# Optimization experiments

Hardware: AMD Instinct MI355X
Metric: run time of the kernel (lower is better)

Reference implementation:

```python
import jax, jax.numpy as jnp
import numpy as np

B, N, F_IN, H, F = 2, 2048, 128, 8, 32  # FH = 256, a has 2F = 64


def setup_inputs() -> dict:
    key = jax.random.key(0)
    k_g, k_x, k_w, k_a = jax.random.split(key, 4)
    # sparse-ish adjacency with self loops (float mask, as in the keras code)
    u = jax.random.uniform(k_g, (B, N, N), dtype=jnp.float32)
    g = jnp.maximum((u < 0.05).astype(jnp.float32), jnp.eye(N, dtype=jnp.float32)[None])
    x = jax.random.normal(k_x, (B, N, F_IN), dtype=jnp.float32)
    w = jax.random.normal(k_w, (F_IN, F * H), dtype=jnp.float32) * (1.0 / np.sqrt(F_IN))
    a = jax.random.normal(k_a, (2 * F,), dtype=jnp.float32) * 0.1
    return {"g": g, "x": x, "w": w, "a": a, "n_heads": H}


def reference(g, x, w, a, n_heads):
    # g: [B,N,N] adjacency, x: [B,N,F_in], w: [F_in, F*H], a: [2F]
    Bd, Nd, _ = g.shape
    Fh = w.shape[1] // n_heads
    # linear transform + split heads: xh[b,n,h,f] == (x@w)[b,n, f + Fh*h]
    xh = jnp.dot(x, w).reshape(Bd, Nd, n_heads, Fh)  # [B,N,H,F]
    a1, a2 = a[:Fh], a[Fh:]
    # concat-attention is linear: score[b,i,j,h] = a1.x_j + a2.x_i
    s_j = jnp.einsum('bnhf,f->bnh', xh, a1)  # contribution of the tiled-over-axis1 copy (_x1 -> node j)
    s_i = jnp.einsum('bnhf,f->bnh', xh, a2)  # contribution of _x2 -> node i
    scores = s_i[:, :, None, :] + s_j[:, None, :, :]  # [B,N,N,H]
    e = jnp.exp(jax.nn.leaky_relu(scores, negative_slope=0.2))
    # normalize by sum over neighbors j masked by adjacency (keepdims like K.sum(..., keepdims=True))
    norm = jnp.sum(e * g[..., None], axis=2, keepdims=True)  # [B,N,1,H]
    return e / norm
```

## Files before the change

kernel.cpp:

```cpp
#include <hip/hip_runtime.h>

constexpr int Bv  = 2;
constexpr int Nv  = 2048;
constexpr int FIN = 128;
constexpr int Hn  = 8;
constexpr int Fv  = 32;
constexpr int NROW = Bv * Nv;
constexpr int S    = NROW * Hn;

typedef float v4f __attribute__((ext_vector_type(4)));

__global__ __launch_bounds__(256) void prep_kernel(
    const float* __restrict__ w, const float* __restrict__ a,
    const float* __restrict__ x, float* __restrict__ pq) {
    __shared__ float wa[2 * FIN * Hn];
    const int tid = threadIdx.x;

    for (int e = tid; e < 2 * FIN * Hn; e += 256) {
        const int which = e >> 10;
        const int k     = (e >> 3) & (FIN - 1);
        const int h     = e & (Hn - 1);
        const float* ap = a + which * Fv;
        const float* wp = w + (size_t)k * (Fv * Hn) + h * Fv;
        float s = 0.f;
        #pragma unroll
        for (int f = 0; f < Fv; ++f) s = fmaf(wp[f], ap[f], s);
        wa[e] = s;
    }
    __syncthreads();

    const int row = blockIdx.x * 32 + (tid >> 3);
    const int h   = tid & (Hn - 1);
    const float* xr = x + (size_t)row * FIN;
    float sj = 0.f, si = 0.f;
    #pragma unroll 4
    for (int k = 0; k < FIN; ++k) {
        const float xv = xr[k];
        sj = fmaf(xv, wa[k * Hn + h], sj);
        si = fmaf(xv, wa[FIN * Hn + k * Hn + h], si);
    }
    const int idx = row * Hn + h;
    pq[idx]         = __expf(sj);
    pq[S + idx]     = __expf(0.2f * sj);
    pq[2 * S + idx] = __expf(si);
    pq[3 * S + idx] = __expf(0.2f * si);
}

__global__ __launch_bounds__(256) void norm_kernel(
    const float* __restrict__ g, const float* __restrict__ pq,
    float* __restrict__ tbl) {
    const int row0 = blockIdx.x * 2;
    const int row1 = row0 + 1;
    const int b    = row0 >> 11;
    const int tid  = threadIdx.x;

    float pi0[Hn], qi0[Hn], pi1[Hn], qi1[Hn];
    #pragma unroll
    for (int h = 0; h < Hn; ++h) {
        pi0[h] = pq[2 * S + row0 * Hn + h];
        qi0[h] = pq[3 * S + row0 * Hn + h];
        pi1[h] = pq[2 * S + row1 * Hn + h];
        qi1[h] = pq[3 * S + row1 * Hn + h];
    }

    const float* __restrict__ g0 = g + (size_t)row0 * Nv;
    const float* __restrict__ g1 = g + (size_t)row1 * Nv;
    const float4* __restrict__ Pj4 = (const float4*)(pq + (size_t)b * Nv * Hn);
    const float4* __restrict__ Qj4 = (const float4*)(pq + S + (size_t)b * Nv * Hn);

    float n0[Hn], n1[Hn];
    #pragma unroll
    for (int h = 0; h < Hn; ++h) { n0[h] = 0.f; n1[h] = 0.f; }

    #pragma unroll 2
    for (int it = 0; it < Nv / 256; ++it) {
        const int j = tid + it * 256;
        const float gv0 = __builtin_nontemporal_load(&g0[j]);
        const float gv1 = __builtin_nontemporal_load(&g1[j]);
        const float4 p0 = Pj4[2 * j], p1 = Pj4[2 * j + 1];
        const float4 q0 = Qj4[2 * j], q1 = Qj4[2 * j + 1];
        const float pj[Hn] = {p0.x, p0.y, p0.z, p0.w, p1.x, p1.y, p1.z, p1.w};
        const float qj[Hn] = {q0.x, q0.y, q0.z, q0.w, q1.x, q1.y, q1.z, q1.w};
        #pragma unroll
        for (int h = 0; h < Hn; ++h) {
            n0[h] = fmaf(gv0, fmaxf(pi0[h] * pj[h], qi0[h] * qj[h]), n0[h]);
            n1[h] = fmaf(gv1, fmaxf(pi1[h] * pj[h], qi1[h] * qj[h]), n1[h]);
        }
    }

    __shared__ float red[4][16];
    const int lane = tid & 63, wv = tid >> 6;
    #pragma unroll
    for (int h = 0; h < Hn; ++h) {
        float v = n0[h];
        #pragma unroll
        for (int off = 32; off > 0; off >>= 1) v += __shfl_down(v, off);
        if (lane == 0) red[wv][h] = v;
    }
    #pragma unroll
    for (int h = 0; h < Hn; ++h) {
        float v = n1[h];
        #pragma unroll
        for (int off = 32; off > 0; off >>= 1) v += __shfl_down(v, off);
        if (lane == 0) red[wv][8 + h] = v;
    }
    __syncthreads();
    if (tid < 16) {
        const int r = tid >> 3, h = tid & 7;
        const int row = row0 + r;
        const float nsum = red[0][tid] + red[1][tid] + red[2][tid] + red[3][tid];
        const float rn = 1.0f / nsum;
        const float piv = pq[2 * S + row * Hn + h];
        const float qiv = pq[3 * S + row * Hn + h];
        tbl[row * 16 + h]     = piv * rn;
        tbl[row * 16 + 8 + h] = qiv * rn;
    }
}

__global__ __launch_bounds__(256) void out_kernel(
    const float* __restrict__ pq, const float* __restrict__ tbl,
    float* __restrict__ out) {
    const int bid  = blockIdx.x;
    const int row  = bid >> 1;
    const int half = bid & 1;
    const int b    = row >> 11;
    const int tid  = threadIdx.x;
    const int hh   = tid & 1;

    const float4 prv = *(const float4*)(tbl + row * 16 + hh * 4);
    const float4 qrv = *(const float4*)(tbl + row * 16 + 8 + hh * 4);

    const float4* __restrict__ Pb = (const float4*)(pq + (size_t)b * Nv * Hn);
    const float4* __restrict__ Qb = (const float4*)(pq + S + (size_t)b * Nv * Hn);
    float* __restrict__ orow = out + (size_t)row * Nv * Hn;

    const int base = half * 2048 + tid;
    #pragma unroll
    for (int it = 0; it < 8; ++it) {
        const int s = base + it * 256;
        const float4 pj = Pb[s];
        const float4 qj = Qb[s];
        v4f o;
        o.x = fmaxf(prv.x * pj.x, qrv.x * qj.x);
        o.y = fmaxf(prv.y * pj.y, qrv.y * qj.y);
        o.z = fmaxf(prv.z * pj.z, qrv.z * qj.z);
        o.w = fmaxf(prv.w * pj.w, qrv.w * qj.w);
        __builtin_nontemporal_store(o, (v4f*)(orow + (size_t)s * 4));
    }
}

extern "C" void kernel_launch(void* const* d_in, const int* in_sizes, int n_in,
                              void* d_out, int out_size, void* d_ws, size_t ws_size,
                              hipStream_t stream) {
    const float* g = (const float*)d_in[0];
    const float* x = (const float*)d_in[1];
    const float* w = (const float*)d_in[2];
    const float* a = (const float*)d_in[3];

    float* pq  = (float*)d_ws;
    float* tbl = pq + 4 * S;
    float* out = (float*)d_out;

    prep_kernel<<<NROW / 32, 256, 0, stream>>>(w, a, x, pq);
    norm_kernel<<<NROW / 2, 256, 0, stream>>>(g, pq, tbl);
    out_kernel<<<NROW * 2, 256, 0, stream>>>(pq, tbl, out);
}
```

Baseline: 91.39 us.

## Compact nonzero adjacency indices in shared memory and gather only neighbors

The normalization kernel now handles one row per block. It first stream-compacts the column indices where the adjacency is nonzero into shared memory, using ballot/popcount and a block-wide prefix. It then sums the attention terms only over those gathered neighbors instead of doing a dense multiply-accumulate over all 2048 columns. This removes about 95% of the arithmetic and of the P/Q table reads, but adds eight block-wide barriers per row and irregular gathers. It also assumes the adjacency values are exactly 0 or 1, since the g weight is no longer multiplied in.

```diff
diff --git a/kernel.cpp b/kernel.cpp
--- a/kernel.cpp
+++ b/kernel.cpp
@@ -49,71 +49,81 @@
 __global__ __launch_bounds__(256) void norm_kernel(
     const float* __restrict__ g, const float* __restrict__ pq,
     float* __restrict__ tbl) {
-    const int row0 = blockIdx.x * 2;
-    const int row1 = row0 + 1;
-    const int b    = row0 >> 11;
+    const int row  = blockIdx.x;
+    const int b    = row >> 11;
     const int tid  = threadIdx.x;
+    const int lane = tid & 63, wv = tid >> 6;
 
-    float pi0[Hn], qi0[Hn], pi1[Hn], qi1[Hn];
+    __shared__ int   idxs[Nv];
+    __shared__ int   wavesum[4];
+    __shared__ int   base_s;
+    __shared__ float red[4][Hn];
+
+    if (tid == 0) base_s = 0;
+    __syncthreads();
+
+    const float* __restrict__ grow = g + (size_t)row * Nv;
+
+    for (int c = 0; c < Nv / 256; ++c) {
+        const int j = c * 256 + tid;
+        const bool pred = grow[j] != 0.f;
+        const unsigned long long m = __ballot(pred);
+        if (lane == 0) wavesum[wv] = __popcll(m);
+        __syncthreads();
+        int woff = base_s;
+        #pragma unroll
+        for (int w2 = 0; w2 < 4; ++w2) if (w2 < wv) woff += wavesum[w2];
+        const int total = wavesum[0] + wavesum[1] + wavesum[2] + wavesum[3];
+        if (pred)
+            idxs[woff + __popcll(m & ((1ull << lane) - 1))] = j;
+        __syncthreads();
+        if (tid == 0) base_s += total;
+    }
+    __syncthreads();
+    const int cnt = base_s;
+
+    float pi[Hn], qi[Hn];
     #pragma unroll
     for (int h = 0; h < Hn; ++h) {
-        pi0[h] = pq[2 * S + row0 * Hn + h];
-        qi0[h] = pq[3 * S + row0 * Hn + h];
-        pi1[h] = pq[2 * S + row1 * Hn + h];
-        qi1[h] = pq[3 * S + row1 * Hn + h];
+        pi[h] = pq[2 * S + row * Hn + h];
+        qi[h] = pq[3 * S + row * Hn + h];
     }
-
-    const float* __restrict__ g0 = g + (size_t)row0 * Nv;
-    const float* __restrict__ g1 = g + (size_t)row1 * Nv;
     const float4* __restrict__ Pj4 = (const float4*)(pq + (size_t)b * Nv * Hn);
     const float4* __restrict__ Qj4 = (const float4*)(pq + S + (size_t)b * Nv * Hn);
 
-    float n0[Hn], n1[Hn];
+    float acc[Hn];
     #pragma unroll
-    for (int h = 0; h < Hn; ++h) { n0[h] = 0.f; n1[h] = 0.f; }
+    for (int h = 0; h < Hn; ++h) acc[h] = 0.f;
 
-    #pragma unroll 2
-    for (int it = 0; it < Nv / 256; ++it) {
-        const int j = tid + it * 256;
-        const float gv0 = __builtin_nontemporal_load(&g0[j]);
-        const float gv1 = __builtin_nontemporal_load(&g1[j]);
-        const float4 p0 = Pj4[2 * j], p1 = Pj4[2 * j + 1];
-        const float4 q0 = Qj4[2 * j], q1 = Qj4[2 * j + 1];
-        const float pj[Hn] = {p0.x, p0.y, p0.z, p0.w, p1.x, p1.y, p1.z, p1.w};
-        const float qj[Hn] = {q0.x, q0.y, q0.z, q0.w, q1.x, q1.y, q1.z, q1.w};
-        #pragma unroll
-        for (int h = 0; h < Hn; ++h) {
-            n0[h] = fmaf(gv0, fmaxf(pi0[h] * pj[h], qi0[h] * qj[h]), n0[h]);
-            n1[h] = fmaf(gv1, fmaxf(pi1[h] * pj[h], qi1[h] * qj[h]), n1[h]);
-        }
+    for (int t = tid; t < cnt; t += 256) {
+        const int jj = idxs[t];
+        const float4 p0 = Pj4[2 * jj], p1 = Pj4[2 * jj + 1];
+        const float4 q0 = Qj4[2 * jj], q1 = Qj4[2 * jj + 1];
+        acc[0] += fmaxf(pi[0] * p0.x, qi[0] * q0.x);
+        acc[1] += fmaxf(pi[1] * p0.y, qi[1] * q0.y);
+        acc[2] += fmaxf(pi[2] * p0.z, qi[2] * q0.z);
+        acc[3] += fmaxf(pi[3] * p0.w, qi[3] * q0.w);
+        acc[4] += fmaxf(pi[4] * p1.x, qi[4] * q1.x);
+        acc[5] += fmaxf(pi[5] * p1.y, qi[5] * q1.y);
+        acc[6] += fmaxf(pi[6] * p1.z, qi[6] * q1.z);
+        acc[7] += fmaxf(pi[7] * p1.w, qi[7] * q1.w);
     }
 
-    __shared__ float red[4][16];
-    const int lane = tid & 63, wv = tid >> 6;
     #pragma unroll
     for (int h = 0; h < Hn; ++h) {
-        float v = n0[h];
+        float v = acc[h];
         #pragma unroll
         for (int off = 32; off > 0; off >>= 1) v += __shfl_down(v, off);
         if (lane == 0) red[wv][h] = v;
     }
-    #pragma unroll
-    for (int h = 0; h < Hn; ++h) {
-        float v = n1[h];
-        #pragma unroll
-        for (int off = 32; off > 0; off >>= 1) v += __shfl_down(v, off);
-        if (lane == 0) red[wv][8 + h] = v;
-    }
     __syncthreads();
-    if (tid < 16) {
-        const int r = tid >> 3, h = tid & 7;
-        const int row = row0 + r;
+    if (tid < Hn) {
         const float nsum = red[0][tid] + red[1][tid] + red[2][tid] + red[3][tid];
         const float rn = 1.0f / nsum;
-        const float piv = pq[2 * S + row * Hn + h];
-        const float qiv = pq[3 * S + row * Hn + h];
-        tbl[row * 16 + h]     = piv * rn;
-        tbl[row * 16 + 8 + h] = qiv * rn;
+        const float piv = pq[2 * S + row * Hn + tid];
+        const float qiv = pq[3 * S + row * Hn + tid];
+        tbl[row * 16 + tid]     = piv * rn;
+        tbl[row * 16 + 8 + tid] = qiv * rn;
     }
 }
 
@@ -162,6 +172,6 @@
     float* out = (float*)d_out;
 
     prep_kernel<<<NROW / 32, 256, 0, stream>>>(w, a, x, pq);
-    norm_kernel<<<NROW / 2, 256, 0, stream>>>(g, pq, tbl);
+    norm_kernel<<<NROW, 256, 0, stream>>>(g, pq, tbl);
     out_kernel<<<NROW * 2, 256, 0, stream>>>(pq, tbl, out);
 }
```

Measured after the change: 87.88 us. 3.8% less time.
